# Kernel optimization log

Hardware: AMD Instinct MI355X
Metric: run time of the kernel (lower is better)

The kernel has to match this reference:

```python
import jax, jax.numpy as jnp
import numpy as np

B, S, HID, HEADS = 1, 512, 1024, 16
HD = HID // HEADS          # 64
LN_EPS = 1e-5
EPS = 1e-8


def setup_inputs() -> dict:
    key = jax.random.key(0)
    ks = jax.random.split(key, 10)
    def w(k, fan_in, shape):
        return (jax.random.normal(k, shape, jnp.float32) / np.sqrt(fan_in)).astype(jnp.float32)
    return {
        "x": jax.random.normal(ks[0], (B, S, HID), jnp.float32),
        "attention_mask": jnp.ones((B, S), jnp.int32),
        "Wq": w(ks[1], HID, (HID, HID)), "bq": jnp.zeros((HID,), jnp.float32),
        "Wk": w(ks[2], HID, (HID, HID)), "bk": jnp.zeros((HID,), jnp.float32),
        "Wv": w(ks[3], HID, (HID, HID)), "bv": jnp.zeros((HID,), jnp.float32),
        "Wo": w(ks[4], HID, (HID, HID)), "bo": jnp.zeros((HID,), jnp.float32),
        "temperature": jnp.ones((1,), jnp.float32),
        "ln_gamma": jnp.ones((HID,), jnp.float32),
        "ln_beta": jnp.zeros((HID,), jnp.float32),
    }


def _forward(x, attention_mask, Wq, bq, Wk, bk, Wv, bv, Wo, bo, temperature, ln_gamma, ln_beta):
    b, s, hid = x.shape
    residual = x
    def proj(W, bias):  # [b,s,hid] -> [b,H,s,hd]
        return (x @ W + bias).reshape(b, s, HEADS, HD).transpose(0, 2, 1, 3)
    Q, K, V = proj(Wq, bq), proj(Wk, bk), proj(Wv, bv)
    # FFT over head_dim -> F = HD//2+1 frequency bins
    Qf = jnp.fft.rfft(Q, axis=-1)
    Kf = jnp.fft.rfft(K, axis=-1)
    Qa, Ka = jnp.abs(Qf), jnp.abs(Kf)
    Qp, Kp = jnp.angle(Qf), jnp.angle(Kf)
    # broadcast to [b,H,Sq,Sk,F]; eps lives inside sqrt (faithful, non-factorized)
    amp_w = jnp.sqrt(Qa[:, :, :, None, :] * Ka[:, :, None, :, :] + EPS)
    phase_align = jnp.cos(Qp[:, :, :, None, :] - Kp[:, :, None, :, :])
    scores = jnp.sum(phase_align * amp_w, axis=-1) * temperature  # [b,H,Sq,Sk]
    mask = attention_mask[:, None, None, :]  # [b,1,1,Sk]
    scores = jnp.where(mask == 0, jnp.float32(-1e9), scores)
    attn = jax.nn.softmax(scores, axis=-1)   # dropout omitted (eval mode)
    out = jnp.einsum('bhqk,bhkd->bhqd', attn, V)
    out = out.transpose(0, 2, 1, 3).reshape(b, s, hid)
    out = out @ Wo + bo
    y = residual + out
    mu = jnp.mean(y, axis=-1, keepdims=True)
    var = jnp.var(y, axis=-1, keepdims=True)
    return (y - mu) / jnp.sqrt(var + LN_EPS) * ln_gamma + ln_beta


def reference(x, attention_mask, Wq, bq, Wk, bk, Wv, bv, Wo, bo, temperature, ln_gamma, ln_beta):
    return _forward(x, attention_mask, Wq, bq, Wk, bk, Wv, bv, Wo, bo,
                    temperature, ln_gamma, ln_beta)
```

## Files before the change

kernel.cpp:

```cpp
#include <hip/hip_runtime.h>
#include <hip/hip_bf16.h>
#include <math.h>

constexpr int SEQ   = 512;
constexpr int HIDC  = 1024;
constexpr int NH    = 16;
constexpr int HDIM  = 64;
constexpr int NFREQ = 33;
constexpr int NFP   = 128;

typedef unsigned short u16;
typedef __bf16 bf16x8 __attribute__((ext_vector_type(8)));
typedef float  f32x4  __attribute__((ext_vector_type(4)));

typedef __attribute__((address_space(3))) void       as3_void;
typedef __attribute__((address_space(1))) const void as1_void;

__device__ __forceinline__ void gload16(const u16* g, u16* l) {
    __builtin_amdgcn_global_load_lds((as1_void*)g, (as3_void*)l, 16, 0, 0);
}

__device__ __forceinline__ float ldin(const void* p, int i, int f32) {
    if (f32) return ((const float*)p)[i];
    return __bfloat162float(((const __hip_bfloat16*)p)[i]);
}

__device__ __forceinline__ u16 f2b(float f) {
    unsigned int u = __builtin_bit_cast(unsigned int, f);
    u += 0x7fffu + ((u >> 16) & 1u);
    return (u16)(u >> 16);
}
__device__ __forceinline__ float b2f(u16 b) {
    return __builtin_bit_cast(float, (unsigned int)b << 16);
}
__device__ __forceinline__ void split2(float f, u16& hi, u16& lo) {
    hi = f2b(f);
    lo = f2b(f - b2f(hi));
}

__global__ void sniff_kernel(const void* w, int* flag) {
    __shared__ int cnt;
    if (threadIdx.x == 0) cnt = 0;
    __syncthreads();
    const unsigned short* h = (const unsigned short*)w;
    int bad = 0;
    for (int i = threadIdx.x; i < 512; i += 256) {
        const unsigned short v = h[i];
        const int ex = (v >> 7) & 0xFF;
        if (ex >= 134) bad++;
    }
    atomicAdd(&cnt, bad);
    __syncthreads();
    if (threadIdx.x == 0) flag[0] = (cnt > 32) ? 1 : 0;
}

__global__ __launch_bounds__(256) void wsplit_kernel(
    const void* __restrict__ W0, const void* __restrict__ W1,
    const void* __restrict__ W2, const void* __restrict__ W3,
    u16* __restrict__ H0, u16* __restrict__ L0,
    u16* __restrict__ H1, u16* __restrict__ L1,
    u16* __restrict__ H2, u16* __restrict__ L2,
    u16* __restrict__ H3, u16* __restrict__ L3,
    const int* __restrict__ flagp)
{
    __shared__ float t[64][65];
    const int F  = *flagp;
    const int mz = blockIdx.z;
    const void* W = (mz == 0) ? W0 : (mz == 1) ? W1 : (mz == 2) ? W2 : W3;
    u16* H = (mz == 0) ? H0 : (mz == 1) ? H1 : (mz == 2) ? H2 : H3;
    u16* L = (mz == 0) ? L0 : (mz == 1) ? L1 : (mz == 2) ? L2 : L3;
    const int n0 = blockIdx.x * 64, k0 = blockIdx.y * 64;
    const int tid = threadIdx.x;

    #pragma unroll
    for (int i = 0; i < 4; ++i) {
        const int item = i * 256 + tid;
        const int r = item >> 4, c4 = (item & 15) * 4;
        if (F) {
            const float4 v = *(const float4*)((const float*)W + (k0 + r) * HIDC + n0 + c4);
            t[r][c4 + 0] = v.x; t[r][c4 + 1] = v.y; t[r][c4 + 2] = v.z; t[r][c4 + 3] = v.w;
        } else {
            #pragma unroll
            for (int j = 0; j < 4; ++j)
                t[r][c4 + j] = ldin(W, (k0 + r) * HIDC + n0 + c4 + j, 0);
        }
    }
    __syncthreads();
    #pragma unroll
    for (int i = 0; i < 4; ++i) {
        const int item = i * 256 + tid;
        const int r = item >> 4, c4 = (item & 15) * 4;
        ushort4 oh, ol;
        u16 h, l;
        split2(t[c4 + 0][r], h, l); oh.x = h; ol.x = l;
        split2(t[c4 + 1][r], h, l); oh.y = h; ol.y = l;
        split2(t[c4 + 2][r], h, l); oh.z = h; ol.z = l;
        split2(t[c4 + 3][r], h, l); oh.w = h; ol.w = l;
        *(ushort4*)&H[(n0 + r) * HIDC + k0 + c4] = oh;
        *(ushort4*)&L[(n0 + r) * HIDC + k0 + c4] = ol;
    }
}

__global__ __launch_bounds__(256) void xsplit_kernel(
    const void* __restrict__ src, u16* __restrict__ hi, u16* __restrict__ lo,
    const int* __restrict__ flagp)
{
    const int F = *flagp;
    const int i = blockIdx.x * 1024 + threadIdx.x * 4;
    float v[4];
    if (F) {
        const float4 f = *(const float4*)((const float*)src + i);
        v[0] = f.x; v[1] = f.y; v[2] = f.z; v[3] = f.w;
    } else {
        #pragma unroll
        for (int j = 0; j < 4; ++j) v[j] = ldin(src, i + j, 0);
    }
    ushort4 oh, ol;
    u16 h, l;
    split2(v[0], h, l); oh.x = h; ol.x = l;
    split2(v[1], h, l); oh.y = h; ol.y = l;
    split2(v[2], h, l); oh.z = h; ol.z = l;
    split2(v[3], h, l); oh.w = h; ol.w = l;
    *(ushort4*)&hi[i] = oh;
    *(ushort4*)&lo[i] = ol;
}

template <int MODE>
__global__ __launch_bounds__(256) void mfma3_gemm_kernel(
    const u16* __restrict__ Ahi, const u16* __restrict__ Alo,
    const u16* __restrict__ B0h, const u16* __restrict__ B0l,
    const u16* __restrict__ B1h, const u16* __restrict__ B1l,
    const u16* __restrict__ B2h, const u16* __restrict__ B2l,
    const void* __restrict__ b0, const void* __restrict__ b1, const void* __restrict__ b2,
    const void* __restrict__ xres,
    float* __restrict__ O0, float* __restrict__ O1, float* __restrict__ O2,
    const int* __restrict__ flagp)
{
    __shared__ __align__(16) u16 smem[2 * 24576];
    const int F    = *flagp;
    const int tid  = threadIdx.x;
    const int lane = tid & 63, wv = tid >> 6;
    const int m0 = blockIdx.y * 64;
    const int n0 = blockIdx.x * 128;

    const u16 *Bh, *Bl; const void* bias; float* Out; int col0;
    if (MODE == 0) {
        const int mat = n0 >> 10;
        col0 = n0 & 1023;
        Bh   = (mat == 0) ? B0h : (mat == 1) ? B1h : B2h;
        Bl   = (mat == 0) ? B0l : (mat == 1) ? B1l : B2l;
        bias = (mat == 0) ? b0  : (mat == 1) ? b1  : b2;
        Out  = (mat == 0) ? O0  : (mat == 1) ? O1  : O2;
    } else {
        col0 = n0; Bh = B0h; Bl = B0l; bias = b0; Out = O0;
    }

    const int rsub = lane >> 3;
    const int gsw  = ((lane & 7) ^ rsub) * 8;
    const u16* pAh[2]; const u16* pAl[2];
    const u16* pBh[4]; const u16* pBl[4];
    int dA[2], dB[4];
    #pragma unroll
    for (int j = 0; j < 2; ++j) {
        const int c = wv * 2 + j;
        pAh[j] = Ahi + (m0 + c * 8 + rsub) * HIDC + gsw;
        pAl[j] = Alo + (m0 + c * 8 + rsub) * HIDC + gsw;
        dA[j]  = c * 512;
    }
    #pragma unroll
    for (int j = 0; j < 4; ++j) {
        const int c = wv * 4 + j;
        pBh[j] = Bh + (col0 + c * 8 + rsub) * HIDC + gsw;
        pBl[j] = Bl + (col0 + c * 8 + rsub) * HIDC + gsw;
        dB[j]  = c * 512;
    }

    int g16[2];
    #pragma unroll
    for (int kc = 0; kc < 2; ++kc) g16[kc] = (((kc * 4) + (lane >> 4)) ^ (lane & 7)) * 8;
    int afo[4], bfo[2];
    #pragma unroll
    for (int mi = 0; mi < 4; ++mi) afo[mi] = (mi * 16 + (lane & 15)) * 64;
    #pragma unroll
    for (int ni = 0; ni < 2; ++ni) bfo[ni] = (wv * 32 + ni * 16 + (lane & 15)) * 64;

    f32x4 zero = {0.f, 0.f, 0.f, 0.f};
    f32x4 acc[4][2];
    #pragma unroll
    for (int mi = 0; mi < 4; ++mi)
        #pragma unroll
        for (int ni = 0; ni < 2; ++ni) acc[mi][ni] = zero;

    #pragma unroll
    for (int j = 0; j < 2; ++j) {
        gload16(pAh[j], smem + dA[j]);
        gload16(pAl[j], smem + 4096 + dA[j]);
    }
    #pragma unroll
    for (int j = 0; j < 4; ++j) {
        gload16(pBh[j], smem + 8192  + dB[j]);
        gload16(pBl[j], smem + 16384 + dB[j]);
    }
    __syncthreads();

    for (int t = 0; t < 16; ++t) {
        const int bo = (t & 1) * 24576;
        if (t < 15) {
            const int bn = 24576 - bo;
            const int k  = (t + 1) * 64;
            #pragma unroll
            for (int j = 0; j < 2; ++j) {
                gload16(pAh[j] + k, smem + bn + dA[j]);
                gload16(pAl[j] + k, smem + bn + 4096 + dA[j]);
            }
            #pragma unroll
            for (int j = 0; j < 4; ++j) {
                gload16(pBh[j] + k, smem + bn + 8192  + dB[j]);
                gload16(pBl[j] + k, smem + bn + 16384 + dB[j]);
            }
        }
        #pragma unroll
        for (int kc = 0; kc < 2; ++kc) {
            bf16x8 ah[4], al[4], bh2[2], bl2[2];
            #pragma unroll
            for (int mi = 0; mi < 4; ++mi) {
                ah[mi] = *(const bf16x8*)(smem + bo +        afo[mi] + g16[kc]);
                al[mi] = *(const bf16x8*)(smem + bo + 4096 + afo[mi] + g16[kc]);
            }
            #pragma unroll
            for (int ni = 0; ni < 2; ++ni) {
                bh2[ni] = *(const bf16x8*)(smem + bo +  8192 + bfo[ni] + g16[kc]);
                bl2[ni] = *(const bf16x8*)(smem + bo + 16384 + bfo[ni] + g16[kc]);
            }
            #pragma unroll
            for (int mi = 0; mi < 4; ++mi)
                #pragma unroll
                for (int ni = 0; ni < 2; ++ni) {
                    acc[mi][ni] = __builtin_amdgcn_mfma_f32_16x16x32_bf16(
                        ah[mi], bh2[ni], acc[mi][ni], 0, 0, 0);
                    acc[mi][ni] = __builtin_amdgcn_mfma_f32_16x16x32_bf16(
                        ah[mi], bl2[ni], acc[mi][ni], 0, 0, 0);
                    acc[mi][ni] = __builtin_amdgcn_mfma_f32_16x16x32_bf16(
                        al[mi], bh2[ni], acc[mi][ni], 0, 0, 0);
                }
        }
        __syncthreads();
    }

    #pragma unroll
    for (int ni = 0; ni < 2; ++ni) {
        const int col = col0 + wv * 32 + ni * 16 + (lane & 15);
        const float bval = ldin(bias, col, F);
        #pragma unroll
        for (int mi = 0; mi < 4; ++mi) {
            const int row0 = m0 + mi * 16 + (lane >> 4) * 4;
            #pragma unroll
            for (int r = 0; r < 4; ++r) {
                const int row = row0 + r;
                float v = acc[mi][ni][r] + bval;
                if (MODE == 1) v += ldin(xres, row * HIDC + col, F);
                Out[row * HIDC + col] = v;
            }
        }
    }
}

__global__ __launch_bounds__(64) void spectral_kernel(
    const float* __restrict__ Q, const float* __restrict__ K,
    u16* __restrict__ Qsh, u16* __restrict__ Qsl,
    u16* __restrict__ Ksh, u16* __restrict__ Ksl)
{
    __shared__ float qv[64];
    __shared__ float tc[64], tsn[64];
    const int unit = blockIdx.x;
    const int sel  = blockIdx.y;
    const int s = unit >> 4, h = unit & 15;
    const float* src = sel ? K : Q;
    u16* dh = sel ? Ksh : Qsh;
    u16* dl = sel ? Ksl : Qsl;
    const int t = threadIdx.x;

    qv[t] = src[s * HIDC + h * HDIM + t];
    float sv, cv;
    sincosf((float)t * (6.283185307179586f / 64.0f), &sv, &cv);
    tc[t] = cv; tsn[t] = sv;
    __syncthreads();

    const int base = (h * SEQ + s) * NFP;
    if (t < NFREQ) {
        float re = 0.0f, im = 0.0f;
        #pragma unroll
        for (int k = 0; k < 64; ++k) {
            const int idx = (t * k) & 63;
            re = fmaf(qv[k], tc[idx], re);
            im = fmaf(qv[k], -tsn[idx], im);
        }
        const float a  = sqrtf(re * re + im * im);
        const float sc = (a > 0.0f) ? rsqrtf(a) : 0.0f;
        u16 hh, ll;
        split2(re * sc, hh, ll);
        dh[base + t] = hh; dl[base + t] = ll;
        split2(im * sc, hh, ll);
        dh[base + NFREQ + t] = hh; dl[base + NFREQ + t] = ll;
    }
    if (t < 62) {
        dh[base + 66 + t] = 0; dl[base + 66 + t] = 0;
    }
}

__global__ __launch_bounds__(256) void vtr_kernel(
    const float* __restrict__ V, u16* __restrict__ VTh, u16* __restrict__ VTl)
{
    __shared__ float t[64][65];
    const int s0 = blockIdx.x * 64, c0 = blockIdx.y * 64;
    const int tid = threadIdx.x;
    #pragma unroll
    for (int i = 0; i < 4; ++i) {
        const int item = i * 256 + tid;
        const int r = item >> 4, c4 = (item & 15) * 4;
        const float4 v = *(const float4*)&V[(s0 + r) * HIDC + c0 + c4];
        t[r][c4 + 0] = v.x; t[r][c4 + 1] = v.y; t[r][c4 + 2] = v.z; t[r][c4 + 3] = v.w;
    }
    __syncthreads();
    #pragma unroll
    for (int i = 0; i < 4; ++i) {
        const int item = i * 256 + tid;
        const int d = item >> 4, s4 = (item & 15) * 4;
        ushort4 oh, ol;
        u16 h, l;
        split2(t[s4 + 0][d], h, l); oh.x = h; ol.x = l;
        split2(t[s4 + 1][d], h, l); oh.y = h; ol.y = l;
        split2(t[s4 + 2][d], h, l); oh.z = h; ol.z = l;
        split2(t[s4 + 3][d], h, l); oh.w = h; ol.w = l;
        *(ushort4*)&VTh[(c0 + d) * SEQ + s0 + s4] = oh;
        *(ushort4*)&VTl[(c0 + d) * SEQ + s0 + s4] = ol;
    }
}

__global__ __launch_bounds__(128) void attn_mfma_kernel(
    const u16* __restrict__ Qsh, const u16* __restrict__ Qsl,
    const u16* __restrict__ Ksh, const u16* __restrict__ Ksl,
    const u16* __restrict__ VTh, const u16* __restrict__ VTl,
    const int* __restrict__ mask, const void* __restrict__ temp_p,
    u16* __restrict__ chi, u16* __restrict__ clo,
    const int* __restrict__ flagp)
{
    __shared__ __align__(16) u16 smem[32768];
    __shared__ int   mask_lds[512];
    __shared__ float l_lds[2][16];

    const int F    = *flagp;
    const int tid  = threadIdx.x;
    const int lane = tid & 63, w = tid >> 6;
    const int hi = lane >> 4, q15 = lane & 15, l7 = lane & 7;
    const int rc = lane >> 4;
    const int h  = blockIdx.y, q0 = blockIdx.x * 32;
    const float temp = ldin(temp_p, 0, F);

    *(int4*)&mask_lds[tid * 4] = *(const int4*)&mask[tid * 4];

    bf16x8 qfh[3], qfl[3];
    {
        const int qrow = (h * SEQ + q0 + w * 16 + q15) * NFP;
        #pragma unroll
        for (int kc = 0; kc < 3; ++kc) {
            qfh[kc] = *(const bf16x8*)(Qsh + qrow + kc * 32 + hi * 8);
            qfl[kc] = *(const bf16x8*)(Qsl + qrow + kc * 32 + hi * 8);
        }
    }

    f32x4 sT[32];
    #pragma unroll
    for (int t = 0; t < 32; ++t) sT[t] = f32x4{0.f, 0.f, 0.f, 0.f};

    constexpr int KH = 0, KL = 16384;
    #pragma unroll
    for (int kt = 0; kt < 4; ++kt) {
        __syncthreads();
        #pragma unroll
        for (int j = 0; j < 16; ++j) {
            const int row = w * 64 + j * 4 + rc;
            const int soff = (h * SEQ + kt * 128 + row) * NFP + ((q15 ^ (row & 7)) * 8);
            gload16(Ksh + soff, smem + KH + (w * 64 + j * 4) * 128);
            gload16(Ksl + soff, smem + KL + (w * 64 + j * 4) * 128);
        }
        __syncthreads();
        #pragma unroll
        for (int tt = 0; tt < 8; ++tt) {
            const int t = kt * 8 + tt;
            #pragma unroll
            for (int kc = 0; kc < 3; ++kc) {
                const int ro = (tt * 16 + q15) * 128 + (((kc * 4 + hi) ^ l7) * 8);
                const bf16x8 ah = *(const bf16x8*)(smem + KH + ro);
                const bf16x8 al = *(const bf16x8*)(smem + KL + ro);
                sT[t] = __builtin_amdgcn_mfma_f32_16x16x32_bf16(ah, qfh[kc], sT[t], 0, 0, 0);
                sT[t] = __builtin_amdgcn_mfma_f32_16x16x32_bf16(ah, qfl[kc], sT[t], 0, 0, 0);
                sT[t] = __builtin_amdgcn_mfma_f32_16x16x32_bf16(al, qfh[kc], sT[t], 0, 0, 0);
            }
        }
    }
    __syncthreads();

    float m = -1e30f;
    #pragma unroll
    for (int t = 0; t < 32; ++t) {
        const int4 mv = *(const int4*)&mask_lds[t * 16 + hi * 4];
        float s;
        s = (mv.x == 0) ? -1e9f : sT[t][0] * temp; sT[t][0] = s; m = fmaxf(m, s);
        s = (mv.y == 0) ? -1e9f : sT[t][1] * temp; sT[t][1] = s; m = fmaxf(m, s);
        s = (mv.z == 0) ? -1e9f : sT[t][2] * temp; sT[t][2] = s; m = fmaxf(m, s);
        s = (mv.w == 0) ? -1e9f : sT[t][3] * temp; sT[t][3] = s; m = fmaxf(m, s);
    }
    m = fmaxf(m, __shfl_xor(m, 16, 64));
    m = fmaxf(m, __shfl_xor(m, 32, 64));
    float sum = 0.0f;
    #pragma unroll
    for (int t = 0; t < 32; ++t) {
        #pragma unroll
        for (int r = 0; r < 4; ++r) {
            const float p = __expf(sT[t][r] - m);
            sT[t][r] = p;
            sum += p;
        }
    }
    sum += __shfl_xor(sum, 16, 64);
    sum += __shfl_xor(sum, 32, 64);
    if (lane < 16) l_lds[w][q15] = sum;

    constexpr int VH = 0, VL = 8192, PB = 16384;
    const int PHo = PB + w * 4352;
    const int PLo = PHo + 2176;
    f32x4 acc[4];
    #pragma unroll
    for (int dt = 0; dt < 4; ++dt) acc[dt] = f32x4{0.f, 0.f, 0.f, 0.f};

    #pragma unroll
    for (int c = 0; c < 4; ++c) {
        __syncthreads();
        #pragma unroll
        for (int j = 0; j < 8; ++j) {
            const int d = w * 32 + j * 4 + rc;
            const int soff = (h * HDIM + d) * SEQ + c * 128 + ((q15 ^ (d & 7)) * 8);
            gload16(VTh + soff, smem + VH + (w * 32 + j * 4) * 128);
            gload16(VTl + soff, smem + VL + (w * 32 + j * 4) * 128);
        }
        #pragma unroll
        for (int tt = 0; tt < 8; ++tt) {
            const int t = c * 8 + tt;
            ushort4 ph, pl;
            u16 hh, ll;
            split2(sT[t][0], hh, ll); ph.x = hh; pl.x = ll;
            split2(sT[t][1], hh, ll); ph.y = hh; pl.y = ll;
            split2(sT[t][2], hh, ll); ph.z = hh; pl.z = ll;
            split2(sT[t][3], hh, ll); ph.w = hh; pl.w = ll;
            const int po = q15 * 136 + tt * 16 + hi * 4;
            *(ushort4*)(smem + PHo + po) = ph;
            *(ushort4*)(smem + PLo + po) = pl;
        }
        __syncthreads();
        #pragma unroll
        for (int dt = 0; dt < 4; ++dt) {
            #pragma unroll
            for (int kc = 0; kc < 4; ++kc) {
                const int po = q15 * 136 + kc * 32 + hi * 8;
                const bf16x8 pfh = *(const bf16x8*)(smem + PHo + po);
                const bf16x8 pfl = *(const bf16x8*)(smem + PLo + po);
                const int vo = (dt * 16 + q15) * 128 + (((kc * 4 + hi) ^ l7) * 8);
                const bf16x8 vfh = *(const bf16x8*)(smem + VH + vo);
                const bf16x8 vfl = *(const bf16x8*)(smem + VL + vo);
                acc[dt] = __builtin_amdgcn_mfma_f32_16x16x32_bf16(pfh, vfh, acc[dt], 0, 0, 0);
                acc[dt] = __builtin_amdgcn_mfma_f32_16x16x32_bf16(pfl, vfh, acc[dt], 0, 0, 0);
                acc[dt] = __builtin_amdgcn_mfma_f32_16x16x32_bf16(pfh, vfl, acc[dt], 0, 0, 0);
            }
        }
    }

    const float4 lv = *(const float4*)&l_lds[w][hi * 4];
    const float lr[4] = {1.0f / lv.x, 1.0f / lv.y, 1.0f / lv.z, 1.0f / lv.w};
    #pragma unroll
    for (int dt = 0; dt < 4; ++dt) {
        #pragma unroll
        for (int r = 0; r < 4; ++r) {
            const float v = acc[dt][r] * lr[r];
            u16 hh, ll;
            split2(v, hh, ll);
            const int row = q0 + w * 16 + hi * 4 + r;
            const int col = h * HDIM + dt * 16 + q15;
            chi[row * HIDC + col] = hh;
            clo[row * HIDC + col] = ll;
        }
    }
}

__global__ __launch_bounds__(256) void ln_kernel(
    const float* __restrict__ Y, const void* __restrict__ gamma,
    const void* __restrict__ beta, void* __restrict__ out,
    const int* __restrict__ flagp)
{
    const int F = *flagp;
    const int row = blockIdx.x, tid = threadIdx.x;
    float v[4];
    float s = 0.0f, s2 = 0.0f;
    #pragma unroll
    for (int j = 0; j < 4; ++j) {
        v[j] = Y[row * HIDC + tid + j * 256];
        s += v[j]; s2 += v[j] * v[j];
    }
    #pragma unroll
    for (int off = 32; off > 0; off >>= 1) {
        s  += __shfl_xor(s, off, 64);
        s2 += __shfl_xor(s2, off, 64);
    }
    __shared__ float wred[4][2];
    const int w = tid >> 6;
    if ((tid & 63) == 0) { wred[w][0] = s; wred[w][1] = s2; }
    __syncthreads();
    s  = wred[0][0] + wred[1][0] + wred[2][0] + wred[3][0];
    s2 = wred[0][1] + wred[1][1] + wred[2][1] + wred[3][1];
    const float mu   = s / (float)HIDC;
    const float var  = s2 / (float)HIDC - mu * mu;
    const float rstd = rsqrtf(var + 1e-5f);
    #pragma unroll
    for (int j = 0; j < 4; ++j) {
        const int c = tid + j * 256;
        const float g = ldin(gamma, c, F), b = ldin(beta, c, F);
        const float r = (v[j] - mu) * rstd * g + b;
        if (F) ((float*)out)[row * HIDC + c] = r;
        else   ((__hip_bfloat16*)out)[row * HIDC + c] = __float2bfloat16(r);
    }
}

extern "C" void kernel_launch(void* const* d_in, const int* in_sizes, int n_in,
                              void* d_out, int out_size, void* d_ws, size_t ws_size,
                              hipStream_t stream) {
    const void* x    = d_in[0];
    const int*  mask = (const int*)d_in[1];
    const void* Wq   = d_in[2];
    const void* bq   = d_in[3];
    const void* Wk   = d_in[4];
    const void* bk   = d_in[5];
    const void* Wv   = d_in[6];
    const void* bv   = d_in[7];
    const void* Wo   = d_in[8];
    const void* bo   = d_in[9];
    const void* temp = d_in[10];
    const void* gam  = d_in[11];
    const void* bet  = d_in[12];

    float* ws   = (float*)d_ws;
    int*   flag = (int*)ws;
    float* Q    = ws + 4;
    float* K    = Q   + SEQ * HIDC;
    float* V    = K   + SEQ * HIDC;
    float* Y    = V   + SEQ * HIDC;
    u16*   xhi  = (u16*)(Y + SEQ * HIDC);
    u16*   xlo  = xhi + SEQ * HIDC;
    u16*   chi  = xlo + SEQ * HIDC;
    u16*   clo  = chi + SEQ * HIDC;
    u16*   Wqh  = clo + SEQ * HIDC;
    u16*   Wql  = Wqh + HIDC * HIDC;
    u16*   Wkh  = Wql + HIDC * HIDC;
    u16*   Wkl  = Wkh + HIDC * HIDC;
    u16*   Wvh  = Wkl + HIDC * HIDC;
    u16*   Wvl  = Wvh + HIDC * HIDC;
    u16*   Woh  = Wvl + HIDC * HIDC;
    u16*   Wol  = Woh + HIDC * HIDC;
    u16*   Qsh  = Wol + HIDC * HIDC;
    u16*   Qsl  = Qsh + NH * SEQ * NFP;
    u16*   Ksh  = Qsl + NH * SEQ * NFP;
    u16*   Ksl  = Ksh + NH * SEQ * NFP;
    u16*   VTh  = Ksl + NH * SEQ * NFP;
    u16*   VTl  = VTh + NH * HDIM * SEQ;

    sniff_kernel<<<1, 256, 0, stream>>>(Wq, flag);

    wsplit_kernel<<<dim3(16, 16, 4), 256, 0, stream>>>(
        Wq, Wk, Wv, Wo, Wqh, Wql, Wkh, Wkl, Wvh, Wvl, Woh, Wol, flag);
    xsplit_kernel<<<512, 256, 0, stream>>>(x, xhi, xlo, flag);

    mfma3_gemm_kernel<0><<<dim3(24, 8), 256, 0, stream>>>(
        xhi, xlo, Wqh, Wql, Wkh, Wkl, Wvh, Wvl,
        bq, bk, bv, nullptr, Q, K, V, flag);

    spectral_kernel<<<dim3(SEQ * NH, 2), 64, 0, stream>>>(Q, K, Qsh, Qsl, Ksh, Ksl);
    vtr_kernel<<<dim3(8, 16), 256, 0, stream>>>(V, VTh, VTl);

    attn_mfma_kernel<<<dim3(SEQ / 32, NH), 128, 0, stream>>>(
        Qsh, Qsl, Ksh, Ksl, VTh, VTl, mask, temp, chi, clo, flag);

    mfma3_gemm_kernel<1><<<dim3(8, 8), 256, 0, stream>>>(
        chi, clo, Woh, Wol, nullptr, nullptr, nullptr, nullptr,
        bo, nullptr, nullptr, x, Y, nullptr, nullptr, flag);

    ln_kernel<<<SEQ, 256, 0, stream>>>(Y, gam, bet, d_out, flag);
}
```

Before: 186.7 us.

## Split attention keys across waves with double-buffered loads; merge weight and x split kernels

The attention kernel now handles 16 queries per block instead of 32, and the block's two waves split the key dimension in halves of 256. Each wave streams its K and V^T tiles through double-buffered LDS with explicit vmcnt waits, so loads overlap the MFMAs. Softmax max and sum are combined across waves through LDS, and the partial PV accumulators are reduced through LDS before normalisation. Separately, the x split is folded into the weight-split kernel as an extra grid z-slice, which removes one launch. This doubles the attention grid and the parallelism, at the cost of extra cross-wave reductions and more Q loads.

```diff
diff --git a/kernel.cpp b/kernel.cpp
--- a/kernel.cpp
+++ b/kernel.cpp
@@ -54,18 +54,46 @@
     if (threadIdx.x == 0) flag[0] = (cnt > 32) ? 1 : 0;
 }
 
-__global__ __launch_bounds__(256) void wsplit_kernel(
+__global__ __launch_bounds__(256) void prep_kernel(
     const void* __restrict__ W0, const void* __restrict__ W1,
     const void* __restrict__ W2, const void* __restrict__ W3,
     u16* __restrict__ H0, u16* __restrict__ L0,
     u16* __restrict__ H1, u16* __restrict__ L1,
     u16* __restrict__ H2, u16* __restrict__ L2,
     u16* __restrict__ H3, u16* __restrict__ L3,
+    const void* __restrict__ xsrc, u16* __restrict__ xhi, u16* __restrict__ xlo,
     const int* __restrict__ flagp)
 {
-    __shared__ float t[64][65];
     const int F  = *flagp;
     const int mz = blockIdx.z;
+
+    if (mz == 4) {
+        const int blk = blockIdx.y * 16 + blockIdx.x;
+        const int i0  = blk * 2048 + threadIdx.x * 8;
+        #pragma unroll
+        for (int g = 0; g < 2; ++g) {
+            const int i = i0 + g * 4;
+            float v[4];
+            if (F) {
+                const float4 f = *(const float4*)((const float*)xsrc + i);
+                v[0] = f.x; v[1] = f.y; v[2] = f.z; v[3] = f.w;
+            } else {
+                #pragma unroll
+                for (int j = 0; j < 4; ++j) v[j] = ldin(xsrc, i + j, 0);
+            }
+            ushort4 oh, ol;
+            u16 h, l;
+            split2(v[0], h, l); oh.x = h; ol.x = l;
+            split2(v[1], h, l); oh.y = h; ol.y = l;
+            split2(v[2], h, l); oh.z = h; ol.z = l;
+            split2(v[3], h, l); oh.w = h; ol.w = l;
+            *(ushort4*)&xhi[i] = oh;
+            *(ushort4*)&xlo[i] = ol;
+        }
+        return;
+    }
+
+    __shared__ float t[64][65];
     const void* W = (mz == 0) ? W0 : (mz == 1) ? W1 : (mz == 2) ? W2 : W3;
     u16* H = (mz == 0) ? H0 : (mz == 1) ? H1 : (mz == 2) ? H2 : H3;
     u16* L = (mz == 0) ? L0 : (mz == 1) ? L1 : (mz == 2) ? L2 : L3;
@@ -99,30 +127,6 @@
         *(ushort4*)&H[(n0 + r) * HIDC + k0 + c4] = oh;
         *(ushort4*)&L[(n0 + r) * HIDC + k0 + c4] = ol;
     }
-}
-
-__global__ __launch_bounds__(256) void xsplit_kernel(
-    const void* __restrict__ src, u16* __restrict__ hi, u16* __restrict__ lo,
-    const int* __restrict__ flagp)
-{
-    const int F = *flagp;
-    const int i = blockIdx.x * 1024 + threadIdx.x * 4;
-    float v[4];
-    if (F) {
-        const float4 f = *(const float4*)((const float*)src + i);
-        v[0] = f.x; v[1] = f.y; v[2] = f.z; v[3] = f.w;
-    } else {
-        #pragma unroll
-        for (int j = 0; j < 4; ++j) v[j] = ldin(src, i + j, 0);
-    }
-    ushort4 oh, ol;
-    u16 h, l;
-    split2(v[0], h, l); oh.x = h; ol.x = l;
-    split2(v[1], h, l); oh.y = h; ol.y = l;
-    split2(v[2], h, l); oh.z = h; ol.z = l;
-    split2(v[3], h, l); oh.w = h; ol.w = l;
-    *(ushort4*)&hi[i] = oh;
-    *(ushort4*)&lo[i] = ol;
 }
 
 template <int MODE>
@@ -347,21 +351,22 @@
 {
     __shared__ __align__(16) u16 smem[32768];
     __shared__ int   mask_lds[512];
-    __shared__ float l_lds[2][16];
+    __shared__ float mpart[2][16], lpart[2][16], l_final[16];
 
     const int F    = *flagp;
     const int tid  = threadIdx.x;
     const int lane = tid & 63, w = tid >> 6;
     const int hi = lane >> 4, q15 = lane & 15, l7 = lane & 7;
-    const int rc = lane >> 4;
-    const int h  = blockIdx.y, q0 = blockIdx.x * 32;
+    const int h  = blockIdx.y, q0 = blockIdx.x * 16;
+    const int k0 = w * 256;
+    const int WB = w * 16384;
     const float temp = ldin(temp_p, 0, F);
 
     *(int4*)&mask_lds[tid * 4] = *(const int4*)&mask[tid * 4];
 
     bf16x8 qfh[3], qfl[3];
     {
-        const int qrow = (h * SEQ + q0 + w * 16 + q15) * NFP;
+        const int qrow = (h * SEQ + q0 + q15) * NFP;
         #pragma unroll
         for (int kc = 0; kc < 3; ++kc) {
             qfh[kc] = *(const bf16x8*)(Qsh + qrow + kc * 32 + hi * 8);
@@ -369,42 +374,67 @@
         }
     }
 
-    f32x4 sT[32];
-    #pragma unroll
-    for (int t = 0; t < 32; ++t) sT[t] = f32x4{0.f, 0.f, 0.f, 0.f};
-
-    constexpr int KH = 0, KL = 16384;
-    #pragma unroll
-    for (int kt = 0; kt < 4; ++kt) {
-        __syncthreads();
-        #pragma unroll
-        for (int j = 0; j < 16; ++j) {
-            const int row = w * 64 + j * 4 + rc;
-            const int soff = (h * SEQ + kt * 128 + row) * NFP + ((q15 ^ (row & 7)) * 8);
-            gload16(Ksh + soff, smem + KH + (w * 64 + j * 4) * 128);
-            gload16(Ksl + soff, smem + KL + (w * 64 + j * 4) * 128);
-        }
-        __syncthreads();
-        #pragma unroll
-        for (int tt = 0; tt < 8; ++tt) {
-            const int t = kt * 8 + tt;
+    const int rc4 = lane >> 4;
+
+    auto stageK = [&](int kt, int b) {
+        const int base = WB + b * 8192;
+        #pragma unroll
+        for (int j = 0; j < 8; ++j) {
+            const int row = j * 4 + rc4;
+            const int gs  = (q15 ^ (row & 7)) * 8;
+            const int so  = (h * SEQ + k0 + kt * 32 + row) * NFP + gs;
+            gload16(Ksh + so, smem + base + j * 512);
+            gload16(Ksl + so, smem + base + 4096 + j * 512);
+        }
+    };
+    auto stageV = [&](int c, int b) {
+        const int base = WB + b * 4096;
+        #pragma unroll
+        for (int j = 0; j < 4; ++j) {
+            const int d  = j * 16 + (lane >> 2);
+            const int gs = ((lane & 3) ^ (d & 3)) * 8;
+            const int so = (h * HDIM + d) * SEQ + k0 + c * 32 + gs;
+            gload16(VTh + so, smem + base + j * 512);
+            gload16(VTl + so, smem + base + 2048 + j * 512);
+        }
+    };
+
+    f32x4 sT[16];
+    #pragma unroll
+    for (int t = 0; t < 16; ++t) sT[t] = f32x4{0.f, 0.f, 0.f, 0.f};
+
+    stageK(0, 0);
+    #pragma unroll
+    for (int kt = 0; kt < 8; ++kt) {
+        if (kt < 7) {
+            stageK(kt + 1, (kt + 1) & 1);
+            asm volatile("s_waitcnt vmcnt(16)" ::: "memory");
+        } else {
+            asm volatile("s_waitcnt vmcnt(0)" ::: "memory");
+        }
+        __builtin_amdgcn_sched_barrier(0);
+        const int base = WB + (kt & 1) * 8192;
+        #pragma unroll
+        for (int tt = 0; tt < 2; ++tt) {
             #pragma unroll
             for (int kc = 0; kc < 3; ++kc) {
                 const int ro = (tt * 16 + q15) * 128 + (((kc * 4 + hi) ^ l7) * 8);
-                const bf16x8 ah = *(const bf16x8*)(smem + KH + ro);
-                const bf16x8 al = *(const bf16x8*)(smem + KL + ro);
-                sT[t] = __builtin_amdgcn_mfma_f32_16x16x32_bf16(ah, qfh[kc], sT[t], 0, 0, 0);
-                sT[t] = __builtin_amdgcn_mfma_f32_16x16x32_bf16(ah, qfl[kc], sT[t], 0, 0, 0);
-                sT[t] = __builtin_amdgcn_mfma_f32_16x16x32_bf16(al, qfh[kc], sT[t], 0, 0, 0);
+                const bf16x8 ah = *(const bf16x8*)(smem + base + ro);
+                const bf16x8 al = *(const bf16x8*)(smem + base + 4096 + ro);
+                sT[kt * 2 + tt] = __builtin_amdgcn_mfma_f32_16x16x32_bf16(ah, qfh[kc], sT[kt * 2 + tt], 0, 0, 0);
+                sT[kt * 2 + tt] = __builtin_amdgcn_mfma_f32_16x16x32_bf16(ah, qfl[kc], sT[kt * 2 + tt], 0, 0, 0);
+                sT[kt * 2 + tt] = __builtin_amdgcn_mfma_f32_16x16x32_bf16(al, qfh[kc], sT[kt * 2 + tt], 0, 0, 0);
             }
         }
     }
-    __syncthreads();
+
+    __builtin_amdgcn_sched_barrier(0);
+    stageV(0, 0);
 
     float m = -1e30f;
     #pragma unroll
-    for (int t = 0; t < 32; ++t) {
-        const int4 mv = *(const int4*)&mask_lds[t * 16 + hi * 4];
+    for (int t = 0; t < 16; ++t) {
+        const int4 mv = *(const int4*)&mask_lds[k0 + t * 16 + hi * 4];
         float s;
         s = (mv.x == 0) ? -1e9f : sT[t][0] * temp; sT[t][0] = s; m = fmaxf(m, s);
         s = (mv.y == 0) ? -1e9f : sT[t][1] * temp; sT[t][1] = s; m = fmaxf(m, s);
@@ -413,78 +443,85 @@
     }
     m = fmaxf(m, __shfl_xor(m, 16, 64));
     m = fmaxf(m, __shfl_xor(m, 32, 64));
+    if (lane < 16) mpart[w][q15] = m;
+    __syncthreads();
+    const float gm = fmaxf(mpart[0][q15], mpart[1][q15]);
     float sum = 0.0f;
     #pragma unroll
-    for (int t = 0; t < 32; ++t) {
+    for (int t = 0; t < 16; ++t) {
         #pragma unroll
         for (int r = 0; r < 4; ++r) {
-            const float p = __expf(sT[t][r] - m);
+            const float p = __expf(sT[t][r] - gm);
             sT[t][r] = p;
             sum += p;
         }
     }
     sum += __shfl_xor(sum, 16, 64);
     sum += __shfl_xor(sum, 32, 64);
-    if (lane < 16) l_lds[w][q15] = sum;
-
-    constexpr int VH = 0, VL = 8192, PB = 16384;
-    const int PHo = PB + w * 4352;
-    const int PLo = PHo + 2176;
+    if (lane < 16) lpart[w][q15] = sum;
+    __syncthreads();
+    if (tid < 16) l_final[tid] = lpart[0][tid] + lpart[1][tid];
+
+    const int PH = WB + 8192, PL = PH + 640;
     f32x4 acc[4];
     #pragma unroll
     for (int dt = 0; dt < 4; ++dt) acc[dt] = f32x4{0.f, 0.f, 0.f, 0.f};
 
     #pragma unroll
-    for (int c = 0; c < 4; ++c) {
-        __syncthreads();
-        #pragma unroll
-        for (int j = 0; j < 8; ++j) {
-            const int d = w * 32 + j * 4 + rc;
-            const int soff = (h * HDIM + d) * SEQ + c * 128 + ((q15 ^ (d & 7)) * 8);
-            gload16(VTh + soff, smem + VH + (w * 32 + j * 4) * 128);
-            gload16(VTl + soff, smem + VL + (w * 32 + j * 4) * 128);
-        }
-        #pragma unroll
-        for (int tt = 0; tt < 8; ++tt) {
-            const int t = c * 8 + tt;
+    for (int c = 0; c < 8; ++c) {
+        if (c < 7) {
+            stageV(c + 1, (c + 1) & 1);
+            asm volatile("s_waitcnt vmcnt(8)" ::: "memory");
+        } else {
+            asm volatile("s_waitcnt vmcnt(0)" ::: "memory");
+        }
+        __builtin_amdgcn_sched_barrier(0);
+        #pragma unroll
+        for (int tt = 0; tt < 2; ++tt) {
+            const int t = c * 2 + tt;
             ushort4 ph, pl;
             u16 hh, ll;
             split2(sT[t][0], hh, ll); ph.x = hh; pl.x = ll;
             split2(sT[t][1], hh, ll); ph.y = hh; pl.y = ll;
             split2(sT[t][2], hh, ll); ph.z = hh; pl.z = ll;
             split2(sT[t][3], hh, ll); ph.w = hh; pl.w = ll;
-            const int po = q15 * 136 + tt * 16 + hi * 4;
-            *(ushort4*)(smem + PHo + po) = ph;
-            *(ushort4*)(smem + PLo + po) = pl;
-        }
-        __syncthreads();
+            const int g  = tt * 2 + (hi >> 1);
+            const int po = q15 * 40 + ((g ^ (q15 & 3)) * 8) + (hi & 1) * 4;
+            *(ushort4*)(smem + PH + po) = ph;
+            *(ushort4*)(smem + PL + po) = pl;
+        }
+        const int vb  = WB + (c & 1) * 4096;
+        const int pro = q15 * 40 + ((hi ^ (q15 & 3)) * 8);
+        const bf16x8 pfh = *(const bf16x8*)(smem + PH + pro);
+        const bf16x8 pfl = *(const bf16x8*)(smem + PL + pro);
         #pragma unroll
         for (int dt = 0; dt < 4; ++dt) {
-            #pragma unroll
-            for (int kc = 0; kc < 4; ++kc) {
-                const int po = q15 * 136 + kc * 32 + hi * 8;
-                const bf16x8 pfh = *(const bf16x8*)(smem + PHo + po);
-                const bf16x8 pfl = *(const bf16x8*)(smem + PLo + po);
-                const int vo = (dt * 16 + q15) * 128 + (((kc * 4 + hi) ^ l7) * 8);
-                const bf16x8 vfh = *(const bf16x8*)(smem + VH + vo);
-                const bf16x8 vfl = *(const bf16x8*)(smem + VL + vo);
-                acc[dt] = __builtin_amdgcn_mfma_f32_16x16x32_bf16(pfh, vfh, acc[dt], 0, 0, 0);
-                acc[dt] = __builtin_amdgcn_mfma_f32_16x16x32_bf16(pfl, vfh, acc[dt], 0, 0, 0);
-                acc[dt] = __builtin_amdgcn_mfma_f32_16x16x32_bf16(pfh, vfl, acc[dt], 0, 0, 0);
-            }
-        }
-    }
-
-    const float4 lv = *(const float4*)&l_lds[w][hi * 4];
-    const float lr[4] = {1.0f / lv.x, 1.0f / lv.y, 1.0f / lv.z, 1.0f / lv.w};
-    #pragma unroll
-    for (int dt = 0; dt < 4; ++dt) {
+            const int vo = (dt * 16 + q15) * 32 + ((hi ^ (q15 & 3)) * 8);
+            const bf16x8 vfh = *(const bf16x8*)(smem + vb + vo);
+            const bf16x8 vfl = *(const bf16x8*)(smem + vb + 2048 + vo);
+            acc[dt] = __builtin_amdgcn_mfma_f32_16x16x32_bf16(pfh, vfh, acc[dt], 0, 0, 0);
+            acc[dt] = __builtin_amdgcn_mfma_f32_16x16x32_bf16(pfl, vfh, acc[dt], 0, 0, 0);
+            acc[dt] = __builtin_amdgcn_mfma_f32_16x16x32_bf16(pfh, vfl, acc[dt], 0, 0, 0);
+        }
+    }
+
+    float* pacc = (float*)(smem + WB + 12288);
+    #pragma unroll
+    for (int dt = 0; dt < 4; ++dt)
+        *(f32x4*)&pacc[(dt * 64 + lane) * 4] = acc[dt];
+    __syncthreads();
+    const float* pa0 = (const float*)(smem + 12288);
+    const float* pa1 = (const float*)(smem + 16384 + 12288);
+    #pragma unroll
+    for (int dd = 0; dd < 2; ++dd) {
+        const int dt = w * 2 + dd;
         #pragma unroll
         for (int r = 0; r < 4; ++r) {
-            const float v = acc[dt][r] * lr[r];
+            const int idx = (dt * 64 + lane) * 4 + r;
+            const float v = (pa0[idx] + pa1[idx]) / l_final[hi * 4 + r];
             u16 hh, ll;
             split2(v, hh, ll);
-            const int row = q0 + w * 16 + hi * 4 + r;
+            const int row = q0 + hi * 4 + r;
             const int col = h * HDIM + dt * 16 + q15;
             chi[row * HIDC + col] = hh;
             clo[row * HIDC + col] = ll;
@@ -574,9 +611,9 @@
 
     sniff_kernel<<<1, 256, 0, stream>>>(Wq, flag);
 
-    wsplit_kernel<<<dim3(16, 16, 4), 256, 0, stream>>>(
-        Wq, Wk, Wv, Wo, Wqh, Wql, Wkh, Wkl, Wvh, Wvl, Woh, Wol, flag);
-    xsplit_kernel<<<512, 256, 0, stream>>>(x, xhi, xlo, flag);
+    prep_kernel<<<dim3(16, 16, 5), 256, 0, stream>>>(
+        Wq, Wk, Wv, Wo, Wqh, Wql, Wkh, Wkl, Wvh, Wvl, Woh, Wol,
+        x, xhi, xlo, flag);
 
     mfma3_gemm_kernel<0><<<dim3(24, 8), 256, 0, stream>>>(
         xhi, xlo, Wqh, Wql, Wkh, Wkl, Wvh, Wvl,
@@ -585,7 +622,7 @@
     spectral_kernel<<<dim3(SEQ * NH, 2), 64, 0, stream>>>(Q, K, Qsh, Qsl, Ksh, Ksl);
     vtr_kernel<<<dim3(8, 16), 256, 0, stream>>>(V, VTh, VTl);
 
-    attn_mfma_kernel<<<dim3(SEQ / 32, NH), 128, 0, stream>>>(
+    attn_mfma_kernel<<<dim3(SEQ / 16, NH), 128, 0, stream>>>(
         Qsh, Qsl, Ksh, Ksl, VTh, VTl, mask, temp, chi, clo, flag);
 
     mfma3_gemm_kernel<1><<<dim3(8, 8), 256, 0, stream>>>(
```

After: 182.1 us. 1.03x faster.
